# Kernel tuning notes

Hardware: AMD Instinct MI355X
Metric: run time of the kernel (lower is better)

Reference implementation:

```python
import jax, jax.numpy as jnp
import numpy as np

NEG_SLOPE = 0.1

def _mlp(x, W, b):
    # Linear + LeakyReLU(0.1), matching MLP(in, out, activation=LeakyReLU(0.1))
    return jax.nn.leaky_relu(jnp.einsum('bnc,cd->bnd', x, W) + b, negative_slope=NEG_SLOPE)

def setup_inputs() -> dict:
    key = jax.random.key(0)
    ks = jax.random.split(key, 5)
    B, N_down, N_up = 4, 16384, 65536
    C_down, C_up, C_out = 256, 128, 128
    x_down = jax.random.normal(ks[0], (B, N_down, C_down), dtype=jnp.float32)
    x_up = jax.random.normal(ks[1], (B, N_up, C_up), dtype=jnp.float32)
    up_idx = jax.random.randint(ks[2], (B, N_up, 1), 0, N_down, dtype=jnp.int64)
    W_lin = jax.random.normal(ks[3], (C_down, C_up), dtype=jnp.float32) * (1.0 / np.sqrt(C_down))
    b_lin = jnp.zeros((C_up,), dtype=jnp.float32)
    W_fus = jax.random.normal(ks[4], (2 * C_up, C_out), dtype=jnp.float32) * (1.0 / np.sqrt(2 * C_up))
    b_fus = jnp.zeros((C_out,), dtype=jnp.float32)
    return {"x_down": x_down, "x_up": x_up, "up_idx": up_idx,
            "W_lin": W_lin, "b_lin": b_lin, "W_fus": W_fus, "b_fus": b_fus}

def reference(x_down, x_up, up_idx, W_lin, b_lin, W_fus, b_fus):
    B, N_up, _ = up_idx.shape
    C_down = x_down.shape[-1]
    # upsampling: gather along point axis, index broadcast over channels
    idx = jnp.broadcast_to(up_idx, (B, N_up, C_down))
    x_g = jnp.take_along_axis(x_down, idx, axis=1)           # [B, N_up, C_down]
    x_lin = _mlp(x_g, W_lin, b_lin)                          # [B, N_up, C_up]
    x_cat = jnp.concatenate([x_up, x_lin], axis=-1)          # [B, N_up, 2*C_up]
    return _mlp(x_cat, W_fus, b_fus)                         # [B, N_up, C_out]
```

## Files before the change

### kernel.cpp

```cpp
#include <hip/hip_runtime.h>
#include <hip/hip_bf16.h>

constexpr int N_DOWN = 16384;
constexpr int N_UP   = 65536;
constexpr int BATCH  = 4;
constexpr int M_BLK  = 64;
constexpr int TS     = 264;

typedef __attribute__((ext_vector_type(8))) short short8;
typedef __attribute__((ext_vector_type(4))) float f32x4;

static __device__ inline unsigned short f2b(float f) {
  __hip_bfloat16 h = __float2bfloat16(f);
  return __builtin_bit_cast(unsigned short, h);
}
static __device__ inline void cvt_store4(__hip_bfloat16* dst, float4 v) {
  ushort4 s;
  s.x = f2b(v.x); s.y = f2b(v.y); s.z = f2b(v.z); s.w = f2b(v.w);
  *(ushort4*)dst = s;
}

__global__ void repack_w(const float* __restrict__ Wl,
                         const float* __restrict__ Wf,
                         __hip_bfloat16* __restrict__ pack) {
  int t = blockIdx.x * 256 + threadIdx.x;
  if (t >= 8192) return;
  int lane  = t & 63;
  int strip = (t >> 6) & 7;
  int kk    = (t >> 9) & 7;
  int w     = t >> 12;
  const float* W = w ? Wf : Wl;
  int q = lane >> 4;
  int l = lane & 15;
  int c = strip * 16 + l;
  short8 vals;
#pragma unroll
  for (int j = 0; j < 8; ++j) {
    int k = kk * 32 + q * 8 + j;
    vals[j] = (short)f2b(W[k * 128 + c]);
  }
  *(short8*)(pack + (size_t)t * 8) = vals;
}

__global__ __launch_bounds__(512, 8)
void mlp1_down(const float* __restrict__ x_down,
               const float* __restrict__ b_lin,
               const __hip_bfloat16* __restrict__ pack,
               __hip_bfloat16* __restrict__ y) {
  __shared__ __hip_bfloat16 T[M_BLK * TS];

  const int tid  = threadIdx.x;
  const int wave = tid >> 6;
  const int lane = tid & 63;
  const int q    = lane >> 4;
  const int l    = lane & 15;
  const int m0   = blockIdx.x * M_BLK;

  {
    const int lr = tid >> 3;
    const int s8 = tid & 7;
    const float* src = x_down + (size_t)(m0 + lr) * 256;
    __hip_bfloat16* dst = T + lr * TS;
#pragma unroll
    for (int j = 0; j < 8; ++j) {
      int c4 = j * 8 + s8;
      float4 v = *(const float4*)(src + c4 * 4);
      cvt_store4(dst + c4 * 4, v);
    }
  }

  short8 B1[8];
#pragma unroll
  for (int kk = 0; kk < 8; ++kk)
    B1[kk] = *(const short8*)(pack + (size_t)((kk * 8 + wave) * 64 + lane) * 8);
  const float bias1 = b_lin[wave * 16 + l];

  __syncthreads();

  f32x4 acc[4];
#pragma unroll
  for (int rg = 0; rg < 4; ++rg) acc[rg] = f32x4{0.f, 0.f, 0.f, 0.f};
#pragma unroll
  for (int kk = 0; kk < 8; ++kk) {
#pragma unroll
    for (int rg = 0; rg < 4; ++rg) {
      short8 a = *(const short8*)(T + (rg * 16 + l) * TS + kk * 32 + q * 8);
      acc[rg] = __builtin_amdgcn_mfma_f32_16x16x32_bf16(a, B1[kk], acc[rg], 0, 0, 0);
    }
  }

#pragma unroll
  for (int rg = 0; rg < 4; ++rg) {
#pragma unroll
    for (int i = 0; i < 4; ++i) {
      float v = acc[rg][i] + bias1;
      v = (v >= 0.f) ? v : 0.1f * v;
      y[(size_t)(m0 + rg * 16 + q * 4 + i) * 128 + wave * 16 + l] = __float2bfloat16(v);
    }
  }
}

__global__ __launch_bounds__(512, 8)
void fused_cat(const float* __restrict__ x_up,
               const int* __restrict__ up_idx,
               const __hip_bfloat16* __restrict__ y,
               const float* __restrict__ b_fus,
               const __hip_bfloat16* __restrict__ pack,
               float* __restrict__ out) {
  __shared__ __hip_bfloat16 T[M_BLK * TS];

  const int tid  = threadIdx.x;
  const int wave = tid >> 6;
  const int lane = tid & 63;
  const int q    = lane >> 4;
  const int l    = lane & 15;
  const int m0   = blockIdx.x * M_BLK;
  const int b    = m0 >> 16;

#pragma unroll
  for (int j = 0; j < 2; ++j) {
    int f = j * 512 + tid;
    int r = f >> 4;
    int c = f & 15;
    int gi = up_idx[m0 + r];
    const __hip_bfloat16* src = y + ((size_t)b * N_DOWN + gi) * 128 + c * 8;
    *(short8*)(T + r * TS + 128 + c * 8) = *(const short8*)src;
  }

#pragma unroll
  for (int j = 0; j < 4; ++j) {
    int f = j * 512 + tid;
    int r = f >> 5;
    int c4 = f & 31;
    float4 v = *(const float4*)(x_up + (size_t)(m0 + r) * 128 + c4 * 4);
    cvt_store4(T + r * TS + c4 * 4, v);
  }

  short8 B2[8];
#pragma unroll
  for (int kk = 0; kk < 8; ++kk)
    B2[kk] = *(const short8*)(pack + (size_t)(4096 + (kk * 8 + wave) * 64 + lane) * 8);
  const float bias2 = b_fus[wave * 16 + l];

  __syncthreads();

  f32x4 acc[4];
#pragma unroll
  for (int rg = 0; rg < 4; ++rg) acc[rg] = f32x4{0.f, 0.f, 0.f, 0.f};
#pragma unroll
  for (int kk = 0; kk < 8; ++kk) {
#pragma unroll
    for (int rg = 0; rg < 4; ++rg) {
      short8 a = *(const short8*)(T + (rg * 16 + l) * TS + kk * 32 + q * 8);
      acc[rg] = __builtin_amdgcn_mfma_f32_16x16x32_bf16(a, B2[kk], acc[rg], 0, 0, 0);
    }
  }

#pragma unroll
  for (int rg = 0; rg < 4; ++rg) {
#pragma unroll
    for (int i = 0; i < 4; ++i) {
      float v = acc[rg][i] + bias2;
      v = (v >= 0.f) ? v : 0.1f * v;
      out[(size_t)(m0 + rg * 16 + q * 4 + i) * 128 + wave * 16 + l] = v;
    }
  }
}

extern "C" void kernel_launch(void* const* d_in, const int* in_sizes, int n_in,
                              void* d_out, int out_size, void* d_ws, size_t ws_size,
                              hipStream_t stream) {
  const float* x_down = (const float*)d_in[0];
  const float* x_up   = (const float*)d_in[1];
  const int*   up_idx = (const int*)d_in[2];
  const float* W_lin  = (const float*)d_in[3];
  const float* b_lin  = (const float*)d_in[4];
  const float* W_fus  = (const float*)d_in[5];
  const float* b_fus  = (const float*)d_in[6];
  float* out = (float*)d_out;

  __hip_bfloat16* pack = (__hip_bfloat16*)d_ws;
  __hip_bfloat16* y    = (__hip_bfloat16*)((char*)d_ws + 131072);

  repack_w<<<32, 256, 0, stream>>>(W_lin, W_fus, pack);
  mlp1_down<<<(BATCH * N_DOWN) / M_BLK, 512, 0, stream>>>(x_down, b_lin, pack, y);
  fused_cat<<<(BATCH * N_UP) / M_BLK, 512, 0, stream>>>(x_up, up_idx, y, b_fus, pack, out);
}
```

Measured before the change: 308.3 us.

## Make fused_cat persistent over four tiles with double-buffered swizzled LDS

Each fused_cat block now handles four consecutive 64-row tiles. Global loads for the next tile (gather of y rows and x_up) are issued before the current tile's MFMA GEMM and written to a second LDS buffer afterwards. The LDS layout changes from a padded stride to an XOR swizzle to avoid bank conflicts. The goal is to hide gather and load latency and to spread weight loading over more work, at the cost of more registers and lower occupancy (launch bounds drop from 8 to 4).

```diff
diff --git a/kernel.cpp b/kernel.cpp
--- a/kernel.cpp
+++ b/kernel.cpp
@@ -6,6 +6,8 @@
 constexpr int BATCH  = 4;
 constexpr int M_BLK  = 64;
 constexpr int TS     = 264;
+constexpr int ITERS  = 4;
+constexpr int GRID_C = (BATCH * N_UP) / M_BLK / ITERS;
 
 typedef __attribute__((ext_vector_type(8))) short short8;
 typedef __attribute__((ext_vector_type(4))) float f32x4;
@@ -100,41 +102,55 @@
   }
 }
 
-__global__ __launch_bounds__(512, 8)
+__global__ __launch_bounds__(512, 4)
 void fused_cat(const float* __restrict__ x_up,
                const int* __restrict__ up_idx,
                const __hip_bfloat16* __restrict__ y,
                const float* __restrict__ b_fus,
                const __hip_bfloat16* __restrict__ pack,
                float* __restrict__ out) {
-  __shared__ __hip_bfloat16 T[M_BLK * TS];
+  __shared__ __hip_bfloat16 T[2][M_BLK * 256];
 
   const int tid  = threadIdx.x;
   const int wave = tid >> 6;
   const int lane = tid & 63;
   const int q    = lane >> 4;
   const int l    = lane & 15;
-  const int m0   = blockIdx.x * M_BLK;
-  const int b    = m0 >> 16;
-
-#pragma unroll
-  for (int j = 0; j < 2; ++j) {
-    int f = j * 512 + tid;
-    int r = f >> 4;
-    int c = f & 15;
-    int gi = up_idx[m0 + r];
-    const __hip_bfloat16* src = y + ((size_t)b * N_DOWN + gi) * 128 + c * 8;
-    *(short8*)(T + r * TS + 128 + c * 8) = *(const short8*)src;
-  }
-
-#pragma unroll
-  for (int j = 0; j < 4; ++j) {
-    int f = j * 512 + tid;
-    int r = f >> 5;
-    int c4 = f & 31;
-    float4 v = *(const float4*)(x_up + (size_t)(m0 + r) * 128 + c4 * 4);
-    cvt_store4(T + r * TS + c4 * 4, v);
-  }
+
+  const int t0 = blockIdx.x * ITERS;
+  const int b  = (t0 * M_BLK) >> 16;
+  const __hip_bfloat16* ybase = y + (size_t)b * N_DOWN * 128;
+
+  const int gr0 = tid >> 4;
+  const int gc  = tid & 15;
+  const int xr  = tid >> 5;
+  const int xc  = tid & 31;
+
+  auto swz = [&](int row, int byte_in_row) -> int {
+    return row * 512 + (byte_in_row ^ ((row & 7) << 4));
+  };
+
+  auto LOAD_IDX = [&](int t, int& ia, int& ib) {
+    const int m0 = t * M_BLK;
+    ia = up_idx[m0 + gr0];
+    ib = up_idx[m0 + gr0 + 32];
+  };
+  auto LOAD_DATA = [&](int t, int ia, int ib, short8 gy[2], float4 xu[4]) {
+    gy[0] = *(const short8*)(ybase + (size_t)ia * 128 + gc * 8);
+    gy[1] = *(const short8*)(ybase + (size_t)ib * 128 + gc * 8);
+    const int m0 = t * M_BLK;
+#pragma unroll
+    for (int j = 0; j < 4; ++j)
+      xu[j] = *(const float4*)(x_up + (size_t)(m0 + j * 16 + xr) * 128 + xc * 4);
+  };
+  auto WRITE_LDS = [&](int buf, short8 gy[2], float4 xu[4]) {
+    char* Tb = (char*)&T[buf][0];
+    *(short8*)(Tb + swz(gr0,      256 + gc * 16)) = gy[0];
+    *(short8*)(Tb + swz(gr0 + 32, 256 + gc * 16)) = gy[1];
+#pragma unroll
+    for (int j = 0; j < 4; ++j)
+      cvt_store4((__hip_bfloat16*)(Tb + swz(j * 16 + xr, xc * 8)), xu[j]);
+  };
 
   short8 B2[8];
 #pragma unroll
@@ -142,28 +158,53 @@
     B2[kk] = *(const short8*)(pack + (size_t)(4096 + (kk * 8 + wave) * 64 + lane) * 8);
   const float bias2 = b_fus[wave * 16 + l];
 
+  auto GEMM_STORE = [&](int buf, int t) {
+    const char* Tb = (const char*)&T[buf][0];
+    f32x4 acc[4];
+#pragma unroll
+    for (int rg = 0; rg < 4; ++rg) acc[rg] = f32x4{0.f, 0.f, 0.f, 0.f};
+#pragma unroll
+    for (int kk = 0; kk < 8; ++kk) {
+#pragma unroll
+      for (int rg = 0; rg < 4; ++rg) {
+        short8 a = *(const short8*)(Tb + swz(rg * 16 + l, kk * 64 + q * 16));
+        acc[rg] = __builtin_amdgcn_mfma_f32_16x16x32_bf16(a, B2[kk], acc[rg], 0, 0, 0);
+      }
+    }
+    const int m0 = t * M_BLK;
+#pragma unroll
+    for (int rg = 0; rg < 4; ++rg) {
+#pragma unroll
+      for (int i = 0; i < 4; ++i) {
+        float v = acc[rg][i] + bias2;
+        v = (v >= 0.f) ? v : 0.1f * v;
+        out[(size_t)(m0 + rg * 16 + q * 4 + i) * 128 + wave * 16 + l] = v;
+      }
+    }
+  };
+
+  int ia, ib, ia2, ib2;
+  short8 gy[2];
+  float4 xu[4];
+
+  LOAD_IDX(t0, ia, ib);
+  LOAD_DATA(t0, ia, ib, gy, xu);
+  WRITE_LDS(0, gy, xu);
+  LOAD_IDX(t0 + 1, ia, ib);
   __syncthreads();
 
-  f32x4 acc[4];
-#pragma unroll
-  for (int rg = 0; rg < 4; ++rg) acc[rg] = f32x4{0.f, 0.f, 0.f, 0.f};
-#pragma unroll
-  for (int kk = 0; kk < 8; ++kk) {
-#pragma unroll
-    for (int rg = 0; rg < 4; ++rg) {
-      short8 a = *(const short8*)(T + (rg * 16 + l) * TS + kk * 32 + q * 8);
-      acc[rg] = __builtin_amdgcn_mfma_f32_16x16x32_bf16(a, B2[kk], acc[rg], 0, 0, 0);
-    }
-  }
-
-#pragma unroll
-  for (int rg = 0; rg < 4; ++rg) {
-#pragma unroll
-    for (int i = 0; i < 4; ++i) {
-      float v = acc[rg][i] + bias2;
-      v = (v >= 0.f) ? v : 0.1f * v;
-      out[(size_t)(m0 + rg * 16 + q * 4 + i) * 128 + wave * 16 + l] = v;
-    }
+#pragma unroll
+  for (int i = 0; i < ITERS; ++i) {
+    if (i + 1 < ITERS) {
+      LOAD_DATA(t0 + i + 1, ia, ib, gy, xu);
+      if (i + 2 < ITERS) LOAD_IDX(t0 + i + 2, ia2, ib2);
+    }
+    GEMM_STORE(i & 1, t0 + i);
+    if (i + 1 < ITERS) {
+      WRITE_LDS((i + 1) & 1, gy, xu);
+      ia = ia2; ib = ib2;
+    }
+    __syncthreads();
   }
 }
 
@@ -184,5 +225,5 @@
 
   repack_w<<<32, 256, 0, stream>>>(W_lin, W_fus, pack);
   mlp1_down<<<(BATCH * N_DOWN) / M_BLK, 512, 0, stream>>>(x_down, b_lin, pack, y);
-  fused_cat<<<(BATCH * N_UP) / M_BLK, 512, 0, stream>>>(x_up, up_idx, y, b_fus, pack, out);
-}
+  fused_cat<<<GRID_C, 512, 0, stream>>>(x_up, up_idx, y, b_fus, pack, out);
+}
```

Result: faster. 302.2 us (-2.0%).

## Remove LDS staging in fused_cat; each wave computes 32 rows from direct global loads

Applied to the files above, without the earlier changes.

The fused concat+MLP kernel no longer stages x_up and the gathered rows in shared memory behind a block barrier. Each wave now owns 32 output rows and all 128 output columns, loading its A fragments straight from global memory (x_up is converted to bf16 in registers) and streaming the weight fragments per MFMA. This drops the LDS round trip and __syncthreads, but every wave reloads the full weight matrix and the A loads are strided across rows, which may make poorer use of cache and memory bandwidth.

```diff
diff --git a/kernel.cpp b/kernel.cpp
--- a/kernel.cpp
+++ b/kernel.cpp
@@ -6,6 +6,9 @@
 constexpr int BATCH  = 4;
 constexpr int M_BLK  = 64;
 constexpr int TS     = 264;
+constexpr int W_ROWS = 32;
+constexpr int NWAVES = (BATCH * N_UP) / W_ROWS;
+constexpr int GRID_C = NWAVES / 4;
 
 typedef __attribute__((ext_vector_type(8))) short short8;
 typedef __attribute__((ext_vector_type(4))) float f32x4;
@@ -18,6 +21,14 @@
   ushort4 s;
   s.x = f2b(v.x); s.y = f2b(v.y); s.z = f2b(v.z); s.w = f2b(v.w);
   *(ushort4*)dst = s;
+}
+static __device__ inline short8 cvt8(float4 v0, float4 v1) {
+  short8 r;
+  r[0] = (short)f2b(v0.x); r[1] = (short)f2b(v0.y);
+  r[2] = (short)f2b(v0.z); r[3] = (short)f2b(v0.w);
+  r[4] = (short)f2b(v1.x); r[5] = (short)f2b(v1.y);
+  r[6] = (short)f2b(v1.z); r[7] = (short)f2b(v1.w);
+  return r;
 }
 
 __global__ void repack_w(const float* __restrict__ Wl,
@@ -100,69 +111,75 @@
   }
 }
 
-__global__ __launch_bounds__(512, 8)
+__global__ __launch_bounds__(256, 4)
 void fused_cat(const float* __restrict__ x_up,
                const int* __restrict__ up_idx,
                const __hip_bfloat16* __restrict__ y,
                const float* __restrict__ b_fus,
                const __hip_bfloat16* __restrict__ pack,
                float* __restrict__ out) {
-  __shared__ __hip_bfloat16 T[M_BLK * TS];
-
   const int tid  = threadIdx.x;
   const int wave = tid >> 6;
   const int lane = tid & 63;
   const int q    = lane >> 4;
   const int l    = lane & 15;
-  const int m0   = blockIdx.x * M_BLK;
-  const int b    = m0 >> 16;
-
-#pragma unroll
-  for (int j = 0; j < 2; ++j) {
-    int f = j * 512 + tid;
-    int r = f >> 4;
-    int c = f & 15;
-    int gi = up_idx[m0 + r];
-    const __hip_bfloat16* src = y + ((size_t)b * N_DOWN + gi) * 128 + c * 8;
-    *(short8*)(T + r * TS + 128 + c * 8) = *(const short8*)src;
-  }
-
-#pragma unroll
-  for (int j = 0; j < 4; ++j) {
-    int f = j * 512 + tid;
-    int r = f >> 5;
-    int c4 = f & 31;
-    float4 v = *(const float4*)(x_up + (size_t)(m0 + r) * 128 + c4 * 4);
-    cvt_store4(T + r * TS + c4 * 4, v);
-  }
-
-  short8 B2[8];
-#pragma unroll
-  for (int kk = 0; kk < 8; ++kk)
-    B2[kk] = *(const short8*)(pack + (size_t)(4096 + (kk * 8 + wave) * 64 + lane) * 8);
-  const float bias2 = b_fus[wave * 16 + l];
-
-  __syncthreads();
-
-  f32x4 acc[4];
-#pragma unroll
-  for (int rg = 0; rg < 4; ++rg) acc[rg] = f32x4{0.f, 0.f, 0.f, 0.f};
-#pragma unroll
-  for (int kk = 0; kk < 8; ++kk) {
-#pragma unroll
-    for (int rg = 0; rg < 4; ++rg) {
-      short8 a = *(const short8*)(T + (rg * 16 + l) * TS + kk * 32 + q * 8);
-      acc[rg] = __builtin_amdgcn_mfma_f32_16x16x32_bf16(a, B2[kk], acc[rg], 0, 0, 0);
-    }
-  }
-
-#pragma unroll
-  for (int rg = 0; rg < 4; ++rg) {
-#pragma unroll
-    for (int i = 0; i < 4; ++i) {
-      float v = acc[rg][i] + bias2;
-      v = (v >= 0.f) ? v : 0.1f * v;
-      out[(size_t)(m0 + rg * 16 + q * 4 + i) * 128 + wave * 16 + l] = v;
+
+  const int gw = blockIdx.x * 4 + wave;
+  const int m0 = gw * W_ROWS;
+  const int b  = m0 >> 16;
+  const __hip_bfloat16* ybase = y + (size_t)b * (N_DOWN * 128);
+  const __hip_bfloat16* packF = pack + 4096 * 8;
+
+  const int i0 = up_idx[m0 + l];
+  const int i1 = up_idx[m0 + 16 + l];
+
+  f32x4 acc[2][8];
+#pragma unroll
+  for (int rg = 0; rg < 2; ++rg)
+#pragma unroll
+    for (int s = 0; s < 8; ++s) acc[rg][s] = f32x4{0.f, 0.f, 0.f, 0.f};
+
+#pragma unroll
+  for (int kk = 0; kk < 4; ++kk) {
+    short8 a[2];
+#pragma unroll
+    for (int rg = 0; rg < 2; ++rg) {
+      const float* p = x_up + (size_t)(m0 + rg * 16 + l) * 128 + kk * 32 + q * 8;
+      float4 v0 = *(const float4*)p;
+      float4 v1 = *(const float4*)(p + 4);
+      a[rg] = cvt8(v0, v1);
+    }
+#pragma unroll
+    for (int s = 0; s < 8; ++s) {
+      short8 Bf = *(const short8*)(packF + (size_t)((kk * 8 + s) * 64 + lane) * 8);
+      acc[0][s] = __builtin_amdgcn_mfma_f32_16x16x32_bf16(a[0], Bf, acc[0][s], 0, 0, 0);
+      acc[1][s] = __builtin_amdgcn_mfma_f32_16x16x32_bf16(a[1], Bf, acc[1][s], 0, 0, 0);
+    }
+  }
+
+#pragma unroll
+  for (int kk = 0; kk < 4; ++kk) {
+    short8 a0 = *(const short8*)(ybase + (size_t)i0 * 128 + kk * 32 + q * 8);
+    short8 a1 = *(const short8*)(ybase + (size_t)i1 * 128 + kk * 32 + q * 8);
+#pragma unroll
+    for (int s = 0; s < 8; ++s) {
+      short8 Bf = *(const short8*)(packF + (size_t)(((kk + 4) * 8 + s) * 64 + lane) * 8);
+      acc[0][s] = __builtin_amdgcn_mfma_f32_16x16x32_bf16(a0, Bf, acc[0][s], 0, 0, 0);
+      acc[1][s] = __builtin_amdgcn_mfma_f32_16x16x32_bf16(a1, Bf, acc[1][s], 0, 0, 0);
+    }
+  }
+
+#pragma unroll
+  for (int s = 0; s < 8; ++s) {
+    const float bs = b_fus[s * 16 + l];
+#pragma unroll
+    for (int rg = 0; rg < 2; ++rg) {
+#pragma unroll
+      for (int i = 0; i < 4; ++i) {
+        float v = acc[rg][s][i] + bs;
+        v = (v >= 0.f) ? v : 0.1f * v;
+        out[(size_t)(m0 + rg * 16 + q * 4 + i) * 128 + s * 16 + l] = v;
+      }
     }
   }
 }
@@ -184,5 +201,5 @@
 
   repack_w<<<32, 256, 0, stream>>>(W_lin, W_fus, pack);
   mlp1_down<<<(BATCH * N_DOWN) / M_BLK, 512, 0, stream>>>(x_down, b_lin, pack, y);
-  fused_cat<<<(BATCH * N_UP) / M_BLK, 512, 0, stream>>>(x_up, up_idx, y, b_fus, pack, out);
-}
+  fused_cat<<<GRID_C, 256, 0, stream>>>(x_up, up_idx, y, b_fus, pack, out);
+}
```

Result: slower. 358.7 us (+16.4%).
